# Kernel tuning notes

Hardware: AMD Instinct MI355X
Metric: run time of the kernel (lower is better)

## Reference

```python
import jax, jax.numpy as jnp
import numpy as np

DIM = 128
NUM_ROT = DIM * (DIM - 1) // 2  # 8128
# Strict upper-triangular pairs in row-major order: i outer, j from i+1 (matches the torch loop)
_PI, _PJ = np.triu_indices(DIM, k=1)


def setup_inputs() -> dict:
    key = jax.random.key(0)
    k1, k2 = jax.random.split(key)
    x = jax.random.normal(k1, (32, 4096, DIM), dtype=jnp.float32)
    angles = jax.random.normal(k2, (NUM_ROT,), dtype=jnp.float32) * 0.01
    bias = jnp.zeros((DIM,), dtype=jnp.float32)
    return {"x": x, "angles": angles, "bias": bias}


def reference(x, angles, bias):
    # Sequential Givens plane rotations applied in pair order (read-after-write chain),
    # expressed as a lax.scan carrying the full vector batch.
    cos_vals = jnp.cos(angles)
    sin_vals = jnp.sin(angles)
    ii = jnp.asarray(_PI, dtype=jnp.int32)
    jj = jnp.asarray(_PJ, dtype=jnp.int32)

    def step(out, cs):
        c, s, i, j = cs
        xi = out[..., i]  # [B, S]
        xj = out[..., j]
        out = out.at[..., i].set(c * xi - s * xj).at[..., j].set(s * xi + c * xj)
        return out, None

    out, _ = jax.lax.scan(step, x, (cos_vals, sin_vals, ii, jj))
    return out + bias
```

## Files before the change

### kernel.cpp

```cpp
#include <hip/hip_runtime.h>
#include <hip/hip_bf16.h>

#define DIM 128
#define G 32

typedef __attribute__((ext_vector_type(4))) float f32x4;
typedef __attribute__((ext_vector_type(8))) short bf16x8;

__device__ const int LOt[G + 1] = {
  0,2,4,6,8,10,13,15,17,19,22,24,27,29,32,35,37,40,43,46,49,53,56,60,64,68,72,77,82,88,95,105,127};
__device__ const int RBt[G + 1] = {
  0,253,502,747,988,1225,1573,1800,2023,2242,2563,2772,3078,3277,3568,3850,4033,4300,4558,4807,
  5047,5353,5572,5850,6112,6358,6588,6853,7093,7348,7600,7875,8128};
__device__ const int AOFFt[G + 1] = {
  0,16384,32512,47888,63016,77416,91576,104916,118024,130456,142664,154112,164928,175432,185332,
  194548,203476,211848,219592,227072,233960,240280,245980,251164,255788,259884,263484,266620,
  269272,271480,273080,274268,274820};
__device__ const int QOFFt[4] = {524288, 540672, 553104, 561476};

__device__ __forceinline__ unsigned short f2bf(float f) {
  union { float f; unsigned int u; } v; v.f = f;
  unsigned int u = v.u;
  return (unsigned short)((u + 0x7FFFu + ((u >> 16) & 1u)) >> 16);
}

__device__ __forceinline__ void load_lds16(const void* src, void* dst) {
  __builtin_amdgcn_global_load_lds((const __attribute__((address_space(1))) void*)src,
                                   (__attribute__((address_space(3))) void*)dst, 16, 0, 0);
}

__global__ __launch_bounds__(256) void k_build(const float* __restrict__ angles,
                                               float* __restrict__ Ascr) {
  __shared__ float  L[DIM * DIM];
  __shared__ float4 cs[256];
  const int g  = blockIdx.x;
  const int lo = LOt[g], n = DIM - lo;
  const int nf = LOt[g + 1] - lo;
  const int P  = (nf + 1) >> 1;
  const int rb = RBt[g], re = RBt[g + 1];
  float* A = Ascr + AOFFt[g];
  const int t = threadIdx.x;

  cs[t] = (float4){1.f, 0.f, 1.f, 0.f};
  __syncthreads();

  for (int r0 = rb + t; r0 < re; r0 += 256) {
    int i = (int)floorf((255.0f - sqrtf(65025.0f - 8.0f * (float)r0)) * 0.5f);
    if (i < 0) i = 0; if (i > 126) i = 126;
    while (127 * (i + 1) - ((i + 1) * i) / 2 <= r0) ++i;
    while (127 * i - (i * (i - 1)) / 2 > r0) --i;
    const int Ti = 127 * i - (i * (i - 1)) / 2;
    const int j  = i + 1 + (r0 - Ti);
    const int fl = i - lo, p = fl >> 1, sec = fl & 1;
    const int f1 = 2 * p, jl = j - lo;
    const int base = p * (n - p);
    float s, c; __sincosf(angles[r0], &s, &c);
    int slot, half;
    if (sec == 0 && jl == f1 + 1) { slot = base; half = 0; }
    else { slot = base + (jl - f1 - 1); half = sec; }
    *((float2*)&cs[slot] + half) = (float2){c, s};
  }
  __syncthreads();

  if (t < n) {
    const int c = t;
    for (int r = 0; r < n; ++r) L[r * n + c] = (r == c) ? 1.0f : 0.0f;
    for (int p = 0; p < P; ++p) {
      const int f1 = 2 * p;
      const int base = p * (n - p);
      const float4 e0 = cs[base];
      float r1 = L[f1 * n + c];
      const float rj = L[(f1 + 1) * n + c];
      float r2 = fmaf(e0.y, r1, e0.x * rj);
      r1 = fmaf(e0.x, r1, -(e0.y * rj));
      #pragma unroll 8
      for (int jl = f1 + 2; jl < n; ++jl) {
        const float4 e = cs[base + (jl - f1 - 1)];
        const float rv = L[jl * n + c];
        const float wv = fmaf(e.y, r1, e.x * rv);
        r1 = fmaf(e.x, r1, -(e.y * rv));
        L[jl * n + c] = fmaf(e.w, r2, e.z * wv);
        r2 = fmaf(e.z, r2, -(e.w * wv));
      }
      L[f1 * n + c] = r1;
      L[(f1 + 1) * n + c] = r2;
    }
  }
  __syncthreads();
  const int np = (n + 3) & ~3;
  if (t < np) {
    for (int r = 0; r < n; ++r)
      A[r * np + t] = (t < n) ? L[r * n + t] : 0.0f;
  }
}

__global__ __launch_bounds__(128) void k_comb1(const float* __restrict__ Ascr,
                                               float* __restrict__ Qscr) {
  __shared__ float x[132];
  const int q = blockIdx.x >> 7, c = blockIdx.x & 127;
  const int loq = LOt[8 * q];
  const int nq  = DIM - loq;
  const int npq = (nq + 3) & ~3;
  if (c >= npq) return;
  const int r = threadIdx.x;
  x[r] = (r == c && c < nq) ? 1.0f : 0.0f;
  if (r < 4) x[128 + r] = 0.0f;
  __syncthreads();
  #pragma unroll 1
  for (int gg = 8 * q; gg < 8 * q + 8; ++gg) {
    const int dg = LOt[gg] - loq;
    const int nb = ((DIM - LOt[gg]) + 3) >> 2;
    float y = x[r];
    if (r >= dg && r < nq) {
      const f32x4* Ar = (const f32x4*)(Ascr + AOFFt[gg] + (r - dg) * (nb << 2));
      float a0 = 0.f, a1 = 0.f, a2 = 0.f, a3 = 0.f;
      #pragma unroll 8
      for (int k = 0; k < nb; ++k) {
        const f32x4 av = Ar[k];
        a0 = fmaf(av[0], x[dg + 4 * k],     a0);
        a1 = fmaf(av[1], x[dg + 4 * k + 1], a1);
        a2 = fmaf(av[2], x[dg + 4 * k + 2], a2);
        a3 = fmaf(av[3], x[dg + 4 * k + 3], a3);
      }
      y = (a0 + a1) + (a2 + a3);
    }
    __syncthreads();
    x[r] = y;
    __syncthreads();
  }
  if (r < nq) Qscr[QOFFt[q] + r * npq + c] = x[r];
}

__global__ __launch_bounds__(128) void k_comb2(const float* __restrict__ Qscr,
                                               unsigned short* __restrict__ Mb) {
  __shared__ float x[132];
  const int c = blockIdx.x, r = threadIdx.x;
  x[r] = (r == c) ? 1.0f : 0.0f;
  if (r < 4) x[128 + r] = 0.0f;
  __syncthreads();
  #pragma unroll 1
  for (int s = 0; s < 4; ++s) {
    const int dg = LOt[8 * s];
    const int np = ((DIM - dg) + 3) & ~3;
    const int nb = np >> 2;
    float y = x[r];
    if (r >= dg) {
      const f32x4* Ar = (const f32x4*)(Qscr + QOFFt[s] + (r - dg) * np);
      float a0 = 0.f, a1 = 0.f, a2 = 0.f, a3 = 0.f;
      #pragma unroll 8
      for (int k = 0; k < nb; ++k) {
        const f32x4 av = Ar[k];
        a0 = fmaf(av[0], x[dg + 4 * k],     a0);
        a1 = fmaf(av[1], x[dg + 4 * k + 1], a1);
        a2 = fmaf(av[2], x[dg + 4 * k + 2], a2);
        a3 = fmaf(av[3], x[dg + 4 * k + 3], a3);
      }
      y = (a0 + a1) + (a2 + a3);
    }
    __syncthreads();
    x[r] = y;
    __syncthreads();
  }
  Mb[r * DIM + c] = f2bf(x[r]);
}

__global__ __launch_bounds__(256) void k_gemm(const float* __restrict__ X,
                                              const float* __restrict__ bias,
                                              const unsigned short* __restrict__ Mb,
                                              float* __restrict__ out) {
  __shared__ unsigned short Bs[16384];
  const int lane = threadIdx.x & 63;
  const int wid  = threadIdx.x >> 6;
  const int l15  = lane & 15, lhi = lane >> 4;
  const int rowbase = blockIdx.x * 128 + wid * 32;

  #pragma unroll
  for (int i = 0; i < 8; ++i) {
    const int chunkbase = (i * 4 + wid) * 64;
    const int d   = chunkbase + lane;
    const int row = d >> 4, pu = d & 15;
    const int usrc = pu ^ (row & 15);
    load_lds16(Mb + row * 128 + usrc * 8, Bs + chunkbase * 8);
  }

  bf16x8 a[2][4];
  #pragma unroll
  for (int mt = 0; mt < 2; ++mt) {
    const float* xp = X + (size_t)(rowbase + mt * 16 + l15) * DIM + lhi * 8;
    #pragma unroll
    for (int kt = 0; kt < 4; ++kt) {
      const f32x4 x0 = *(const f32x4*)(xp + kt * 32);
      const f32x4 x1 = *(const f32x4*)(xp + kt * 32 + 4);
      bf16x8 av;
      av[0] = (short)f2bf(x0[0]); av[1] = (short)f2bf(x0[1]);
      av[2] = (short)f2bf(x0[2]); av[3] = (short)f2bf(x0[3]);
      av[4] = (short)f2bf(x1[0]); av[5] = (short)f2bf(x1[1]);
      av[6] = (short)f2bf(x1[2]); av[7] = (short)f2bf(x1[3]);
      a[mt][kt] = av;
    }
  }

  f32x4 acc[2][8];
  #pragma unroll
  for (int m = 0; m < 2; ++m)
    #pragma unroll
    for (int n = 0; n < 8; ++n) acc[m][n] = (f32x4){0.f, 0.f, 0.f, 0.f};

  __syncthreads();

  #pragma unroll
  for (int kt = 0; kt < 4; ++kt) {
    const int pu = ((kt * 4 + lhi) ^ l15) * 8;
    #pragma unroll
    for (int n = 0; n < 8; ++n) {
      const bf16x8 b = *(const bf16x8*)&Bs[(l15 + 16 * n) * 128 + pu];
      acc[0][n] = __builtin_amdgcn_mfma_f32_16x16x32_bf16(b, a[0][kt], acc[0][n], 0, 0, 0);
      acc[1][n] = __builtin_amdgcn_mfma_f32_16x16x32_bf16(b, a[1][kt], acc[1][n], 0, 0, 0);
    }
  }

  #pragma unroll
  for (int n = 0; n < 8; ++n) {
    const f32x4 bv = *(const f32x4*)(bias + 16 * n + lhi * 4);
    #pragma unroll
    for (int mt = 0; mt < 2; ++mt) {
      const f32x4 v = acc[mt][n] + bv;
      *(f32x4*)(out + (size_t)(rowbase + mt * 16 + l15) * DIM + 16 * n + lhi * 4) = v;
    }
  }
}

extern "C" void kernel_launch(void* const* d_in, const int* in_sizes, int n_in,
                              void* d_out, int out_size, void* d_ws, size_t ws_size,
                              hipStream_t stream) {
  const float* x      = (const float*)d_in[0];
  const float* angles = (const float*)d_in[1];
  const float* bias   = (const float*)d_in[2];
  float* out  = (float*)d_out;
  float* scr  = (float*)d_out;
  unsigned short* Mb = (unsigned short*)d_ws;

  k_build<<<G, 256, 0, stream>>>(angles, scr);
  k_comb1<<<512, 128, 0, stream>>>(scr, scr);
  k_comb2<<<128, 128, 0, stream>>>(scr, Mb);
  k_gemm<<<1024, 256, 0, stream>>>(x, bias, Mb, out);
}
```

Measured before the change: 93.95 us.

## Fuse matrix-build stages into one cooperative kernel and halve GEMM grid

Merges the three prep kernels (per-group Givens block build, first combine, second combine) into one cooperative kernel of 256 blocks, separated by grid-wide syncs, so two kernel launches and their gaps go away. Each block now handles two combine tasks, one per 128-thread half. The GEMM launches 512 blocks that each process two 128-row tiles, which amortises loading the rotation matrix into LDS over twice the rows. The cost is the grid.sync overhead, a cooperative launch that requires every block to be resident at once, and higher register pressure in the GEMM from holding both tiles' A fragments.

```diff
diff --git a/kernel.cpp b/kernel.cpp
--- a/kernel.cpp
+++ b/kernel.cpp
@@ -1,5 +1,8 @@
 #include <hip/hip_runtime.h>
 #include <hip/hip_bf16.h>
+#include <hip/hip_cooperative_groups.h>
+
+namespace cg = cooperative_groups;
 
 #define DIM 128
 #define G 32
@@ -29,139 +32,151 @@
                                    (__attribute__((address_space(3))) void*)dst, 16, 0, 0);
 }
 
-__global__ __launch_bounds__(256) void k_build(const float* __restrict__ angles,
-                                               float* __restrict__ Ascr) {
+__global__ __launch_bounds__(256) void k_prep(const float* __restrict__ angles,
+                                              float* __restrict__ scr,
+                                              unsigned short* __restrict__ Mb) {
   __shared__ float  L[DIM * DIM];
   __shared__ float4 cs[256];
-  const int g  = blockIdx.x;
-  const int lo = LOt[g], n = DIM - lo;
-  const int nf = LOt[g + 1] - lo;
-  const int P  = (nf + 1) >> 1;
-  const int rb = RBt[g], re = RBt[g + 1];
-  float* A = Ascr + AOFFt[g];
-  const int t = threadIdx.x;
-
-  cs[t] = (float4){1.f, 0.f, 1.f, 0.f};
-  __syncthreads();
-
-  for (int r0 = rb + t; r0 < re; r0 += 256) {
-    int i = (int)floorf((255.0f - sqrtf(65025.0f - 8.0f * (float)r0)) * 0.5f);
-    if (i < 0) i = 0; if (i > 126) i = 126;
-    while (127 * (i + 1) - ((i + 1) * i) / 2 <= r0) ++i;
-    while (127 * i - (i * (i - 1)) / 2 > r0) --i;
-    const int Ti = 127 * i - (i * (i - 1)) / 2;
-    const int j  = i + 1 + (r0 - Ti);
-    const int fl = i - lo, p = fl >> 1, sec = fl & 1;
-    const int f1 = 2 * p, jl = j - lo;
-    const int base = p * (n - p);
-    float s, c; __sincosf(angles[r0], &s, &c);
-    int slot, half;
-    if (sec == 0 && jl == f1 + 1) { slot = base; half = 0; }
-    else { slot = base + (jl - f1 - 1); half = sec; }
-    *((float2*)&cs[slot] + half) = (float2){c, s};
-  }
-  __syncthreads();
-
-  if (t < n) {
-    const int c = t;
-    for (int r = 0; r < n; ++r) L[r * n + c] = (r == c) ? 1.0f : 0.0f;
-    for (int p = 0; p < P; ++p) {
-      const int f1 = 2 * p;
+  const int t   = threadIdx.x;
+  const int bid = blockIdx.x;
+  cg::grid_group grid = cg::this_grid();
+
+  if (bid < G) {
+    const int g  = bid;
+    const int lo = LOt[g], n = DIM - lo;
+    const int nf = LOt[g + 1] - lo;
+    const int P  = (nf + 1) >> 1;
+    const int rb = RBt[g], re = RBt[g + 1];
+    float* A = scr + AOFFt[g];
+
+    cs[t] = (float4){1.f, 0.f, 1.f, 0.f};
+    __syncthreads();
+    for (int r0 = rb + t; r0 < re; r0 += 256) {
+      int i = (int)floorf((255.0f - sqrtf(65025.0f - 8.0f * (float)r0)) * 0.5f);
+      if (i < 0) i = 0; if (i > 126) i = 126;
+      while (127 * (i + 1) - ((i + 1) * i) / 2 <= r0) ++i;
+      while (127 * i - (i * (i - 1)) / 2 > r0) --i;
+      const int Ti = 127 * i - (i * (i - 1)) / 2;
+      const int j  = i + 1 + (r0 - Ti);
+      const int fl = i - lo, p = fl >> 1, sec = fl & 1;
+      const int f1 = 2 * p, jl = j - lo;
       const int base = p * (n - p);
-      const float4 e0 = cs[base];
-      float r1 = L[f1 * n + c];
-      const float rj = L[(f1 + 1) * n + c];
-      float r2 = fmaf(e0.y, r1, e0.x * rj);
-      r1 = fmaf(e0.x, r1, -(e0.y * rj));
-      #pragma unroll 8
-      for (int jl = f1 + 2; jl < n; ++jl) {
-        const float4 e = cs[base + (jl - f1 - 1)];
-        const float rv = L[jl * n + c];
-        const float wv = fmaf(e.y, r1, e.x * rv);
-        r1 = fmaf(e.x, r1, -(e.y * rv));
-        L[jl * n + c] = fmaf(e.w, r2, e.z * wv);
-        r2 = fmaf(e.z, r2, -(e.w * wv));
-      }
-      L[f1 * n + c] = r1;
-      L[(f1 + 1) * n + c] = r2;
-    }
-  }
-  __syncthreads();
-  const int np = (n + 3) & ~3;
-  if (t < np) {
-    for (int r = 0; r < n; ++r)
-      A[r * np + t] = (t < n) ? L[r * n + t] : 0.0f;
-  }
-}
-
-__global__ __launch_bounds__(128) void k_comb1(const float* __restrict__ Ascr,
-                                               float* __restrict__ Qscr) {
-  __shared__ float x[132];
-  const int q = blockIdx.x >> 7, c = blockIdx.x & 127;
-  const int loq = LOt[8 * q];
-  const int nq  = DIM - loq;
-  const int npq = (nq + 3) & ~3;
-  if (c >= npq) return;
-  const int r = threadIdx.x;
-  x[r] = (r == c && c < nq) ? 1.0f : 0.0f;
-  if (r < 4) x[128 + r] = 0.0f;
-  __syncthreads();
-  #pragma unroll 1
-  for (int gg = 8 * q; gg < 8 * q + 8; ++gg) {
-    const int dg = LOt[gg] - loq;
-    const int nb = ((DIM - LOt[gg]) + 3) >> 2;
-    float y = x[r];
-    if (r >= dg && r < nq) {
-      const f32x4* Ar = (const f32x4*)(Ascr + AOFFt[gg] + (r - dg) * (nb << 2));
-      float a0 = 0.f, a1 = 0.f, a2 = 0.f, a3 = 0.f;
-      #pragma unroll 8
-      for (int k = 0; k < nb; ++k) {
-        const f32x4 av = Ar[k];
-        a0 = fmaf(av[0], x[dg + 4 * k],     a0);
-        a1 = fmaf(av[1], x[dg + 4 * k + 1], a1);
-        a2 = fmaf(av[2], x[dg + 4 * k + 2], a2);
-        a3 = fmaf(av[3], x[dg + 4 * k + 3], a3);
-      }
-      y = (a0 + a1) + (a2 + a3);
-    }
-    __syncthreads();
-    x[r] = y;
-    __syncthreads();
-  }
-  if (r < nq) Qscr[QOFFt[q] + r * npq + c] = x[r];
-}
-
-__global__ __launch_bounds__(128) void k_comb2(const float* __restrict__ Qscr,
-                                               unsigned short* __restrict__ Mb) {
-  __shared__ float x[132];
-  const int c = blockIdx.x, r = threadIdx.x;
-  x[r] = (r == c) ? 1.0f : 0.0f;
-  if (r < 4) x[128 + r] = 0.0f;
-  __syncthreads();
-  #pragma unroll 1
-  for (int s = 0; s < 4; ++s) {
-    const int dg = LOt[8 * s];
-    const int np = ((DIM - dg) + 3) & ~3;
-    const int nb = np >> 2;
-    float y = x[r];
-    if (r >= dg) {
-      const f32x4* Ar = (const f32x4*)(Qscr + QOFFt[s] + (r - dg) * np);
-      float a0 = 0.f, a1 = 0.f, a2 = 0.f, a3 = 0.f;
-      #pragma unroll 8
-      for (int k = 0; k < nb; ++k) {
-        const f32x4 av = Ar[k];
-        a0 = fmaf(av[0], x[dg + 4 * k],     a0);
-        a1 = fmaf(av[1], x[dg + 4 * k + 1], a1);
-        a2 = fmaf(av[2], x[dg + 4 * k + 2], a2);
-        a3 = fmaf(av[3], x[dg + 4 * k + 3], a3);
-      }
-      y = (a0 + a1) + (a2 + a3);
-    }
-    __syncthreads();
-    x[r] = y;
-    __syncthreads();
-  }
-  Mb[r * DIM + c] = f2bf(x[r]);
+      float s, c; __sincosf(angles[r0], &s, &c);
+      int slot, half;
+      if (sec == 0 && jl == f1 + 1) { slot = base; half = 0; }
+      else { slot = base + (jl - f1 - 1); half = sec; }
+      *((float2*)&cs[slot] + half) = (float2){c, s};
+    }
+    __syncthreads();
+
+    if (t < n) {
+      const int c = t;
+      for (int r = 0; r < n; ++r) L[r * n + c] = (r == c) ? 1.0f : 0.0f;
+      for (int p = 0; p < P; ++p) {
+        const int f1 = 2 * p;
+        const int base = p * (n - p);
+        const float4 e0 = cs[base];
+        float r1 = L[f1 * n + c];
+        const float rj = L[(f1 + 1) * n + c];
+        float r2 = fmaf(e0.y, r1, e0.x * rj);
+        r1 = fmaf(e0.x, r1, -(e0.y * rj));
+        #pragma unroll 8
+        for (int jl = f1 + 2; jl < n; ++jl) {
+          const float4 e = cs[base + (jl - f1 - 1)];
+          const float rv = L[jl * n + c];
+          const float wv = fmaf(e.y, r1, e.x * rv);
+          r1 = fmaf(e.x, r1, -(e.y * rv));
+          L[jl * n + c] = fmaf(e.w, r2, e.z * wv);
+          r2 = fmaf(e.z, r2, -(e.w * wv));
+        }
+        L[f1 * n + c] = r1;
+        L[(f1 + 1) * n + c] = r2;
+      }
+    }
+    __syncthreads();
+    const int np = (n + 3) & ~3;
+    if (t < np) {
+      for (int r = 0; r < n; ++r)
+        A[r * np + t] = (t < n) ? L[r * n + t] : 0.0f;
+    }
+  }
+  __threadfence();
+  grid.sync();
+  __threadfence();
+
+  {
+    const int half = t >> 7, r = t & 127;
+    const int task = bid * 2 + half;
+    const int q = task >> 7, c = task & 127;
+    const int loq = LOt[8 * q];
+    const int nq  = DIM - loq;
+    const int npq = (nq + 3) & ~3;
+    float* x = L + half * 136;
+    x[r] = (r == c && c < nq) ? 1.0f : 0.0f;
+    if (r < 4) x[128 + r] = 0.0f;
+    __syncthreads();
+    #pragma unroll 1
+    for (int gg = 8 * q; gg < 8 * q + 8; ++gg) {
+      const int dg = LOt[gg] - loq;
+      const int nb = ((DIM - LOt[gg]) + 3) >> 2;
+      float y = x[r];
+      if (r >= dg && r < nq) {
+        const f32x4* Ar = (const f32x4*)(scr + AOFFt[gg] + (r - dg) * (nb << 2));
+        float a0 = 0.f, a1 = 0.f, a2 = 0.f, a3 = 0.f;
+        #pragma unroll 8
+        for (int k = 0; k < nb; ++k) {
+          const f32x4 av = Ar[k];
+          a0 = fmaf(av[0], x[dg + 4 * k],     a0);
+          a1 = fmaf(av[1], x[dg + 4 * k + 1], a1);
+          a2 = fmaf(av[2], x[dg + 4 * k + 2], a2);
+          a3 = fmaf(av[3], x[dg + 4 * k + 3], a3);
+        }
+        y = (a0 + a1) + (a2 + a3);
+      }
+      __syncthreads();
+      x[r] = y;
+      __syncthreads();
+    }
+    if (r < nq && c < npq) scr[QOFFt[q] + r * npq + c] = x[r];
+  }
+  __threadfence();
+  grid.sync();
+  __threadfence();
+
+  {
+    const int half = t >> 7, r = t & 127;
+    const int task = bid * 2 + half;
+    if (bid >= 64) return;
+    const int c = task;
+    float* x = L + half * 136;
+    x[r] = (r == c) ? 1.0f : 0.0f;
+    if (r < 4) x[128 + r] = 0.0f;
+    __syncthreads();
+    #pragma unroll 1
+    for (int s = 0; s < 4; ++s) {
+      const int dg = LOt[8 * s];
+      const int np = ((DIM - dg) + 3) & ~3;
+      const int nb = np >> 2;
+      float y = x[r];
+      if (r >= dg) {
+        const f32x4* Ar = (const f32x4*)(scr + QOFFt[s] + (r - dg) * np);
+        float a0 = 0.f, a1 = 0.f, a2 = 0.f, a3 = 0.f;
+        #pragma unroll 8
+        for (int k = 0; k < nb; ++k) {
+          const f32x4 av = Ar[k];
+          a0 = fmaf(av[0], x[dg + 4 * k],     a0);
+          a1 = fmaf(av[1], x[dg + 4 * k + 1], a1);
+          a2 = fmaf(av[2], x[dg + 4 * k + 2], a2);
+          a3 = fmaf(av[3], x[dg + 4 * k + 3], a3);
+        }
+        y = (a0 + a1) + (a2 + a3);
+      }
+      __syncthreads();
+      x[r] = y;
+      __syncthreads();
+    }
+    Mb[r * DIM + c] = f2bf(x[r]);
+  }
 }
 
 __global__ __launch_bounds__(256) void k_gemm(const float* __restrict__ X,
@@ -172,7 +187,6 @@
   const int lane = threadIdx.x & 63;
   const int wid  = threadIdx.x >> 6;
   const int l15  = lane & 15, lhi = lane >> 4;
-  const int rowbase = blockIdx.x * 128 + wid * 32;
 
   #pragma unroll
   for (int i = 0; i < 8; ++i) {
@@ -183,49 +197,57 @@
     load_lds16(Mb + row * 128 + usrc * 8, Bs + chunkbase * 8);
   }
 
-  bf16x8 a[2][4];
+  bf16x8 a[2][2][4];
   #pragma unroll
-  for (int mt = 0; mt < 2; ++mt) {
-    const float* xp = X + (size_t)(rowbase + mt * 16 + l15) * DIM + lhi * 8;
+  for (int it = 0; it < 2; ++it) {
+    const int rowbase = (blockIdx.x + it * 512) * 128 + wid * 32;
+    #pragma unroll
+    for (int mt = 0; mt < 2; ++mt) {
+      const float* xp = X + (size_t)(rowbase + mt * 16 + l15) * DIM + lhi * 8;
+      #pragma unroll
+      for (int kt = 0; kt < 4; ++kt) {
+        const f32x4 x0 = *(const f32x4*)(xp + kt * 32);
+        const f32x4 x1 = *(const f32x4*)(xp + kt * 32 + 4);
+        bf16x8 av;
+        av[0] = (short)f2bf(x0[0]); av[1] = (short)f2bf(x0[1]);
+        av[2] = (short)f2bf(x0[2]); av[3] = (short)f2bf(x0[3]);
+        av[4] = (short)f2bf(x1[0]); av[5] = (short)f2bf(x1[1]);
+        av[6] = (short)f2bf(x1[2]); av[7] = (short)f2bf(x1[3]);
+        a[it][mt][kt] = av;
+      }
+    }
+  }
+
+  __syncthreads();
+
+  #pragma unroll
+  for (int it = 0; it < 2; ++it) {
+    const int rowbase = (blockIdx.x + it * 512) * 128 + wid * 32;
+    f32x4 acc[2][8];
+    #pragma unroll
+    for (int m = 0; m < 2; ++m)
+      #pragma unroll
+      for (int n = 0; n < 8; ++n) acc[m][n] = (f32x4){0.f, 0.f, 0.f, 0.f};
+
     #pragma unroll
     for (int kt = 0; kt < 4; ++kt) {
-      const f32x4 x0 = *(const f32x4*)(xp + kt * 32);
-      const f32x4 x1 = *(const f32x4*)(xp + kt * 32 + 4);
-      bf16x8 av;
-      av[0] = (short)f2bf(x0[0]); av[1] = (short)f2bf(x0[1]);
-      av[2] = (short)f2bf(x0[2]); av[3] = (short)f2bf(x0[3]);
-      av[4] = (short)f2bf(x1[0]); av[5] = (short)f2bf(x1[1]);
-      av[6] = (short)f2bf(x1[2]); av[7] = (short)f2bf(x1[3]);
-      a[mt][kt] = av;
-    }
-  }
-
-  f32x4 acc[2][8];
-  #pragma unroll
-  for (int m = 0; m < 2; ++m)
-    #pragma unroll
-    for (int n = 0; n < 8; ++n) acc[m][n] = (f32x4){0.f, 0.f, 0.f, 0.f};
-
-  __syncthreads();
-
-  #pragma unroll
-  for (int kt = 0; kt < 4; ++kt) {
-    const int pu = ((kt * 4 + lhi) ^ l15) * 8;
+      const int pu = ((kt * 4 + lhi) ^ l15) * 8;
+      #pragma unroll
+      for (int n = 0; n < 8; ++n) {
+        const bf16x8 b = *(const bf16x8*)&Bs[(l15 + 16 * n) * 128 + pu];
+        acc[0][n] = __builtin_amdgcn_mfma_f32_16x16x32_bf16(b, a[it][0][kt], acc[0][n], 0, 0, 0);
+        acc[1][n] = __builtin_amdgcn_mfma_f32_16x16x32_bf16(b, a[it][1][kt], acc[1][n], 0, 0, 0);
+      }
+    }
+
     #pragma unroll
     for (int n = 0; n < 8; ++n) {
-      const bf16x8 b = *(const bf16x8*)&Bs[(l15 + 16 * n) * 128 + pu];
-      acc[0][n] = __builtin_amdgcn_mfma_f32_16x16x32_bf16(b, a[0][kt], acc[0][n], 0, 0, 0);
-      acc[1][n] = __builtin_amdgcn_mfma_f32_16x16x32_bf16(b, a[1][kt], acc[1][n], 0, 0, 0);
-    }
-  }
-
-  #pragma unroll
-  for (int n = 0; n < 8; ++n) {
-    const f32x4 bv = *(const f32x4*)(bias + 16 * n + lhi * 4);
-    #pragma unroll
-    for (int mt = 0; mt < 2; ++mt) {
-      const f32x4 v = acc[mt][n] + bv;
-      *(f32x4*)(out + (size_t)(rowbase + mt * 16 + l15) * DIM + 16 * n + lhi * 4) = v;
+      const f32x4 bv = *(const f32x4*)(bias + 16 * n + lhi * 4);
+      #pragma unroll
+      for (int mt = 0; mt < 2; ++mt) {
+        const f32x4 v = acc[mt][n] + bv;
+        *(f32x4*)(out + (size_t)(rowbase + mt * 16 + l15) * DIM + 16 * n + lhi * 4) = v;
+      }
     }
   }
 }
@@ -240,8 +262,7 @@
   float* scr  = (float*)d_out;
   unsigned short* Mb = (unsigned short*)d_ws;
 
-  k_build<<<G, 256, 0, stream>>>(angles, scr);
-  k_comb1<<<512, 128, 0, stream>>>(scr, scr);
-  k_comb2<<<128, 128, 0, stream>>>(scr, Mb);
-  k_gemm<<<1024, 256, 0, stream>>>(x, bias, Mb, out);
-}
+  void* args[] = {(void*)&angles, (void*)&scr, (void*)&Mb};
+  hipLaunchCooperativeKernel((const void*)k_prep, dim3(256), dim3(256), args, 0, stream);
+  k_gemm<<<512, 256, 0, stream>>>(x, bias, Mb, out);
+}
```

Result: slower. 217.4 us (+131.4%).

## Make GEMM blocks loop over four row tiles with register prefetch of next tile

Applied to the files above, without the earlier changes.

The GEMM kernel now launches 256 blocks, and each block processes four consecutive 128-row tiles. The bf16 matrix is loaded into LDS once per block rather than once per tile. Raw fp32 activations for the next tile are loaded into registers while the current tile's MFMAs run, overlapping global loads with compute. This raises register pressure and lowers grid parallelism (256 blocks for a 256-CU part), which may reduce the latency hiding that came from more resident waves.

```diff
diff --git a/kernel.cpp b/kernel.cpp
--- a/kernel.cpp
+++ b/kernel.cpp
@@ -164,6 +164,8 @@
   Mb[r * DIM + c] = f2bf(x[r]);
 }
 
+#define TILES 4
+#define GEMM_BLOCKS 256
 __global__ __launch_bounds__(256) void k_gemm(const float* __restrict__ X,
                                               const float* __restrict__ bias,
                                               const unsigned short* __restrict__ Mb,
@@ -172,7 +174,7 @@
   const int lane = threadIdx.x & 63;
   const int wid  = threadIdx.x >> 6;
   const int l15  = lane & 15, lhi = lane >> 4;
-  const int rowbase = blockIdx.x * 128 + wid * 32;
+  const int tile0 = blockIdx.x * TILES;
 
   #pragma unroll
   for (int i = 0; i < 8; ++i) {
@@ -183,49 +185,79 @@
     load_lds16(Mb + row * 128 + usrc * 8, Bs + chunkbase * 8);
   }
 
-  bf16x8 a[2][4];
+  f32x4 raw[2][4][2];
+  {
+    const int rowbase = tile0 * 128 + wid * 32;
+    #pragma unroll
+    for (int mt = 0; mt < 2; ++mt) {
+      const float* xp = X + (size_t)(rowbase + mt * 16 + l15) * DIM + lhi * 8;
+      #pragma unroll
+      for (int kt = 0; kt < 4; ++kt) {
+        raw[mt][kt][0] = *(const f32x4*)(xp + kt * 32);
+        raw[mt][kt][1] = *(const f32x4*)(xp + kt * 32 + 4);
+      }
+    }
+  }
+
+  __syncthreads();
+
   #pragma unroll
-  for (int mt = 0; mt < 2; ++mt) {
-    const float* xp = X + (size_t)(rowbase + mt * 16 + l15) * DIM + lhi * 8;
+  for (int it = 0; it < TILES; ++it) {
+    const int rowbase = (tile0 + it) * 128 + wid * 32;
+
+    bf16x8 a[2][4];
+    #pragma unroll
+    for (int mt = 0; mt < 2; ++mt)
+      #pragma unroll
+      for (int kt = 0; kt < 4; ++kt) {
+        const f32x4 x0 = raw[mt][kt][0];
+        const f32x4 x1 = raw[mt][kt][1];
+        bf16x8 av;
+        av[0] = (short)f2bf(x0[0]); av[1] = (short)f2bf(x0[1]);
+        av[2] = (short)f2bf(x0[2]); av[3] = (short)f2bf(x0[3]);
+        av[4] = (short)f2bf(x1[0]); av[5] = (short)f2bf(x1[1]);
+        av[6] = (short)f2bf(x1[2]); av[7] = (short)f2bf(x1[3]);
+        a[mt][kt] = av;
+      }
+
+    if (it < TILES - 1) {
+      const int nrb = (tile0 + it + 1) * 128 + wid * 32;
+      #pragma unroll
+      for (int mt = 0; mt < 2; ++mt) {
+        const float* xp = X + (size_t)(nrb + mt * 16 + l15) * DIM + lhi * 8;
+        #pragma unroll
+        for (int kt = 0; kt < 4; ++kt) {
+          raw[mt][kt][0] = *(const f32x4*)(xp + kt * 32);
+          raw[mt][kt][1] = *(const f32x4*)(xp + kt * 32 + 4);
+        }
+      }
+    }
+
+    f32x4 acc[2][8];
+    #pragma unroll
+    for (int m = 0; m < 2; ++m)
+      #pragma unroll
+      for (int n = 0; n < 8; ++n) acc[m][n] = (f32x4){0.f, 0.f, 0.f, 0.f};
+
     #pragma unroll
     for (int kt = 0; kt < 4; ++kt) {
-      const f32x4 x0 = *(const f32x4*)(xp + kt * 32);
-      const f32x4 x1 = *(const f32x4*)(xp + kt * 32 + 4);
-      bf16x8 av;
-      av[0] = (short)f2bf(x0[0]); av[1] = (short)f2bf(x0[1]);
-      av[2] = (short)f2bf(x0[2]); av[3] = (short)f2bf(x0[3]);
-      av[4] = (short)f2bf(x1[0]); av[5] = (short)f2bf(x1[1]);
-      av[6] = (short)f2bf(x1[2]); av[7] = (short)f2bf(x1[3]);
-      a[mt][kt] = av;
-    }
-  }
-
-  f32x4 acc[2][8];
-  #pragma unroll
-  for (int m = 0; m < 2; ++m)
-    #pragma unroll
-    for (int n = 0; n < 8; ++n) acc[m][n] = (f32x4){0.f, 0.f, 0.f, 0.f};
-
-  __syncthreads();
-
-  #pragma unroll
-  for (int kt = 0; kt < 4; ++kt) {
-    const int pu = ((kt * 4 + lhi) ^ l15) * 8;
+      const int pu = ((kt * 4 + lhi) ^ l15) * 8;
+      #pragma unroll
+      for (int n = 0; n < 8; ++n) {
+        const bf16x8 b = *(const bf16x8*)&Bs[(l15 + 16 * n) * 128 + pu];
+        acc[0][n] = __builtin_amdgcn_mfma_f32_16x16x32_bf16(b, a[0][kt], acc[0][n], 0, 0, 0);
+        acc[1][n] = __builtin_amdgcn_mfma_f32_16x16x32_bf16(b, a[1][kt], acc[1][n], 0, 0, 0);
+      }
+    }
+
     #pragma unroll
     for (int n = 0; n < 8; ++n) {
-      const bf16x8 b = *(const bf16x8*)&Bs[(l15 + 16 * n) * 128 + pu];
-      acc[0][n] = __builtin_amdgcn_mfma_f32_16x16x32_bf16(b, a[0][kt], acc[0][n], 0, 0, 0);
-      acc[1][n] = __builtin_amdgcn_mfma_f32_16x16x32_bf16(b, a[1][kt], acc[1][n], 0, 0, 0);
-    }
-  }
-
-  #pragma unroll
-  for (int n = 0; n < 8; ++n) {
-    const f32x4 bv = *(const f32x4*)(bias + 16 * n + lhi * 4);
-    #pragma unroll
-    for (int mt = 0; mt < 2; ++mt) {
-      const f32x4 v = acc[mt][n] + bv;
-      *(f32x4*)(out + (size_t)(rowbase + mt * 16 + l15) * DIM + 16 * n + lhi * 4) = v;
+      const f32x4 bv = *(const f32x4*)(bias + 16 * n + lhi * 4);
+      #pragma unroll
+      for (int mt = 0; mt < 2; ++mt) {
+        const f32x4 v = acc[mt][n] + bv;
+        *(f32x4*)(out + (size_t)(rowbase + mt * 16 + l15) * DIM + 16 * n + lhi * 4) = v;
+      }
     }
   }
 }
@@ -243,5 +275,5 @@
   k_build<<<G, 256, 0, stream>>>(angles, scr);
   k_comb1<<<512, 128, 0, stream>>>(scr, scr);
   k_comb2<<<128, 128, 0, stream>>>(scr, Mb);
-  k_gemm<<<1024, 256, 0, stream>>>(x, bias, Mb, out);
-}
+  k_gemm<<<GEMM_BLOCKS, 256, 0, stream>>>(x, bias, Mb, out);
+}
```

After: 94.53 us. Within noise of the previous version (+0.6%).
